# Optimization experiments

Measured on AMD Instinct MI355X. Metric: run time of the kernel, lower is better.

The kernel has to match this reference:

```python
import jax, jax.numpy as jnp
import numpy as np

H = 256   # hidden_dim
K = 4     # number of z_layer Linears
T = 8192  # number of permutation trees (Z-nodes) in the batch
C = 16    # children (leaf indices) per tree
N = 200000  # rows in batch.x node-feature table


def setup_inputs() -> dict:
    key = jax.random.key(0)
    ks = jax.random.split(key, 6)
    x = jax.random.normal(ks[0], (N, H), dtype=jnp.float32)
    leaf_idx = jax.random.randint(ks[1], (T, C), 0, N)
    # z_layer: k Linears (y = x @ W + b), z_final_layer: one Linear
    scale = 1.0 / np.sqrt(H)
    Wz = jax.random.uniform(ks[2], (K, H, H), dtype=jnp.float32, minval=-scale, maxval=scale)
    bz = jax.random.uniform(ks[3], (K, H), dtype=jnp.float32, minval=-scale, maxval=scale)
    Wzf = jax.random.uniform(ks[4], (H, H), dtype=jnp.float32, minval=-scale, maxval=scale)
    bzf = jax.random.uniform(ks[5], (H,), dtype=jnp.float32, minval=-scale, maxval=scale)
    return {"x": x, "Wz": Wz, "bz": bz, "Wzf": Wzf, "bzf": bzf, "leaf_idx": leaf_idx}


def reference(x, Wz, bz, Wzf, bzf, leaf_idx):
    # Batched z_layer_fn over T trees, each a Z-node over C leaf children.
    data = x[leaf_idx]                                   # [T, C, H] gather (fetch_or_produce)
    # k parallel Linears: [K, T, C, H]
    after = jnp.einsum('tch,khd->ktcd', data, Wz) + bz[:, None, None, :]
    # embedding_k[torch.roll(arange(C), shifts=k)] == roll(embedding_k, k, axis=children)
    k = after.shape[0]
    rolled_sum = after[0]
    for i in range(1, k):  # tiny fixed loop over k layers
        rolled_sum = rolled_sum + jnp.roll(after[i], i, axis=1)
    h = jax.nn.elu(rolled_sum)                           # [T, C, H]
    h = jnp.einsum('tch,hd->tcd', h, Wzf) + bzf          # z_final_layer
    out = jax.nn.elu(jnp.sum(h, axis=1))                 # sum over children, ELU -> [T, H]
    return out
```

## Files before the change

kernel.cpp:

```cpp
#include <hip/hip_runtime.h>
#include <hip/hip_bf16.h>
#include <stdint.h>

#define TREES 8192
#define HID   256
#define CH    16
#define KL    4
#define G     8
#define LDSS  264

typedef short bf16x8 __attribute__((ext_vector_type(8)));
typedef float f32x4  __attribute__((ext_vector_type(4)));

__device__ __forceinline__ unsigned short f2bf(float f) {
    unsigned u = __builtin_bit_cast(unsigned, f);
    u += 0x7FFFu + ((u >> 16) & 1u);
    return (unsigned short)(u >> 16);
}
__device__ __forceinline__ float elu1(float x) {
    return x > 0.f ? x : (__expf(x) - 1.f);
}

__global__ void prep_transpose(const float* __restrict__ Wz,
                               const float* __restrict__ Wzf,
                               unsigned short* __restrict__ WzT,
                               unsigned short* __restrict__ WzfT) {
    __shared__ unsigned short ts[64][65];
    const int k  = blockIdx.z;
    const int h0 = blockIdx.x * 64;
    const int d0 = blockIdx.y * 64;
    const float* src = (k < KL) ? (Wz + (k << 16)) : Wzf;
    unsigned short* dst = (k < KL) ? (WzT + (k << 16)) : WzfT;
    const int tid = threadIdx.x;
    const int jc  = tid & 63;
    #pragma unroll
    for (int r = 0; r < 16; ++r) {
        int i = r * 4 + (tid >> 6);
        ts[jc][i] = f2bf(src[(h0 + i) * HID + d0 + jc]);
    }
    __syncthreads();
    #pragma unroll
    for (int r = 0; r < 16; ++r) {
        int jl = r * 4 + (tid >> 6);
        dst[(d0 + jl) * HID + h0 + jc] = ts[jl][jc];
    }
}

__global__ void prep_bzsum(const float* __restrict__ bz, float* __restrict__ bzsum) {
    int d = threadIdx.x;
    float s = 0.f;
    #pragma unroll
    for (int k = 0; k < KL; ++k) s += bz[k * HID + d];
    bzsum[d] = s;
}

__global__ __launch_bounds__(256, 2) void ptree_kernel(
    const float* __restrict__ x,
    const int* __restrict__ leaf,
    const float* __restrict__ bzf,
    const unsigned short* __restrict__ WzT,
    const unsigned short* __restrict__ WzfT,
    const float* __restrict__ bzsum,
    float* __restrict__ out,
    int nrows)
{
    __shared__ __align__(16) unsigned short sh[G][CH][LDSS];
    __shared__ __align__(16) unsigned short hs[CH][LDSS];
    const int tid  = threadIdx.x;
    const int lane = tid & 63;
    const int wave = tid >> 6;
    const int t0   = blockIdx.x * G;
    const int ncol = lane & 15;
    const int quad = lane >> 4;

    #pragma unroll
    for (int i = 0; i < (G * CH * 32) / 256; ++i) {
        int cid = i * 256 + tid;
        int g   = cid >> 9;
        int row = (cid >> 5) & 15;
        int ch  = cid & 31;
        int idx = leaf[(t0 + g) * CH + row];
        idx = (idx >= 0 && idx < nrows) ? idx : 0;
        const float* src = x + (size_t)idx * HID + ch * 8;
        float4 v0 = *(const float4*)src;
        float4 v1 = *(const float4*)(src + 4);
        union { uint4 u4; unsigned short s[8]; } U;
        U.s[0] = f2bf(v0.x); U.s[1] = f2bf(v0.y);
        U.s[2] = f2bf(v0.z); U.s[3] = f2bf(v0.w);
        U.s[4] = f2bf(v1.x); U.s[5] = f2bf(v1.y);
        U.s[6] = f2bf(v1.z); U.s[7] = f2bf(v1.w);
        *(uint4*)&sh[g][row][ch * 8] = U.u4;
    }

    float bzs[4], bzfv[4];
    #pragma unroll
    for (int nt = 0; nt < 4; ++nt) {
        bzs[nt]  = bzsum[wave * 64 + nt * 16 + ncol];
        bzfv[nt] = bzf[wave * 64 + nt * 16 + ncol];
    }

    __syncthreads();

    f32x4 acc1[G][4];
    #pragma unroll
    for (int g = 0; g < G; ++g)
        #pragma unroll
        for (int nt = 0; nt < 4; ++nt) acc1[g][nt] = f32x4{0.f, 0.f, 0.f, 0.f};

    const unsigned short* wz_base = WzT + (wave * 64 + ncol) * HID + quad * 8;
    bf16x8 bc[4], bn[4];
    #pragma unroll
    for (int nt = 0; nt < 4; ++nt)
        bc[nt] = *(const bf16x8*)(wz_base + nt * 16 * HID);

    #pragma unroll 2
    for (int s = 0; s < KL * 8; ++s) {
        const int sn = (s < KL * 8 - 1) ? s + 1 : s;
        const unsigned short* pn = wz_base + (sn >> 3) * 65536 + (sn & 7) * 32;
        #pragma unroll
        for (int nt = 0; nt < 4; ++nt)
            bn[nt] = *(const bf16x8*)(pn + nt * 16 * HID);
        const int k    = s >> 3;
        const int kt   = s & 7;
        const int arow = (ncol - k) & 15;
        #pragma unroll
        for (int g = 0; g < G; ++g) {
            bf16x8 a = *(const bf16x8*)&sh[g][arow][kt * 32 + quad * 8];
            #pragma unroll
            for (int nt = 0; nt < 4; ++nt)
                acc1[g][nt] = __builtin_amdgcn_mfma_f32_16x16x32_bf16(a, bc[nt], acc1[g][nt], 0, 0, 0);
        }
        #pragma unroll
        for (int nt = 0; nt < 4; ++nt) bc[nt] = bn[nt];
    }

    #pragma unroll
    for (int g = 0; g < G; ++g)
        #pragma unroll
        for (int nt = 0; nt < 4; ++nt) {
            float s = 0.f;
            #pragma unroll
            for (int r = 0; r < 4; ++r) s += elu1(acc1[g][nt][r] + bzs[nt]);
            s += __shfl_xor(s, 16);
            s += __shfl_xor(s, 32);
            if (quad == 0) hs[g][wave * 64 + nt * 16 + ncol] = f2bf(s);
        }

    __syncthreads();

    f32x4 acc2[4];
    #pragma unroll
    for (int nt = 0; nt < 4; ++nt) acc2[nt] = f32x4{0.f, 0.f, 0.f, 0.f};

    const unsigned short* wzf_base = WzfT + (wave * 64 + ncol) * HID + quad * 8;
    #pragma unroll 2
    for (int kt = 0; kt < 8; ++kt) {
        bf16x8 a = *(const bf16x8*)&hs[ncol & 7][kt * 32 + quad * 8];
        if (ncol >= 8) a = bf16x8{0, 0, 0, 0, 0, 0, 0, 0};
        #pragma unroll
        for (int nt = 0; nt < 4; ++nt) {
            bf16x8 b = *(const bf16x8*)(wzf_base + nt * 16 * HID + kt * 32);
            acc2[nt] = __builtin_amdgcn_mfma_f32_16x16x32_bf16(a, b, acc2[nt], 0, 0, 0);
        }
    }

    #pragma unroll
    for (int nt = 0; nt < 4; ++nt)
        #pragma unroll
        for (int r = 0; r < 4; ++r) {
            int tree = quad * 4 + r;
            if (tree < G) {
                float v = elu1(acc2[nt][r] + 16.f * bzfv[nt]);
                out[(size_t)(t0 + tree) * HID + wave * 64 + nt * 16 + ncol] = v;
            }
        }
}

extern "C" void kernel_launch(void* const* d_in, const int* in_sizes, int n_in,
                              void* d_out, int out_size, void* d_ws, size_t ws_size,
                              hipStream_t stream) {
    (void)out_size; (void)ws_size;
    const void* p_x = nullptr; const void* p_Wz = nullptr; const void* p_bz = nullptr;
    const void* p_Wzf = nullptr; const void* p_bzf = nullptr; const void* p_leaf = nullptr;
    for (int i = 0; i < n_in; ++i) {
        switch (in_sizes[i]) {
            case 200000 * 256:   p_x    = d_in[i]; break;
            case KL * 256 * 256: p_Wz   = d_in[i]; break;
            case KL * 256:       p_bz   = d_in[i]; break;
            case 256 * 256:      p_Wzf  = d_in[i]; break;
            case 256:            p_bzf  = d_in[i]; break;
            case TREES * CH:     p_leaf = d_in[i]; break;
        }
    }
    const float* x    = (const float*)p_x;
    const float* Wz   = (const float*)p_Wz;
    const float* bz   = (const float*)p_bz;
    const float* Wzf  = (const float*)p_Wzf;
    const float* bzf  = (const float*)p_bzf;
    const int*   leaf = (const int*)p_leaf;

    unsigned short* WzT  = (unsigned short*)d_ws;
    unsigned short* WzfT = WzT + KL * HID * HID;
    float*          bzsum = (float*)(WzfT + HID * HID);

    dim3 tg(4, 4, KL + 1);
    prep_transpose<<<tg, 256, 0, stream>>>(Wz, Wzf, WzT, WzfT);
    prep_bzsum<<<1, HID, 0, stream>>>(bz, bzsum);
    ptree_kernel<<<TREES / G, 256, 0, stream>>>(x, leaf, bzf, WzT, WzfT, bzsum,
                                                (float*)d_out, 200000);
}
```

Before: 349.5 us.

## Halve trees per block, alias hidden buffer into gather LDS, batch gather loads

Cuts trees per block from 8 to 4 and raises the launch-bounds occupancy hint to 4 blocks per CU. The stage-two hidden buffer now reuses the gather LDS region, which needs an extra barrier after the first MFMA loop. The gather first loads all leaf indices, then issues global loads in batches of four before converting them to bf16, giving more memory-level parallelism. In exchange, each block now reads the weights for only half as many trees, doubling total weight traffic from L2, and the second GEMM uses only 4 of its 16 MFMA rows.

```diff
diff --git a/kernel.cpp b/kernel.cpp
--- a/kernel.cpp
+++ b/kernel.cpp
@@ -6,7 +6,7 @@
 #define HID   256
 #define CH    16
 #define KL    4
-#define G     8
+#define G     4
 #define LDSS  264
 
 typedef short bf16x8 __attribute__((ext_vector_type(8)));
@@ -54,7 +54,7 @@
     bzsum[d] = s;
 }
 
-__global__ __launch_bounds__(256, 2) void ptree_kernel(
+__global__ __launch_bounds__(256, 4) void ptree_kernel(
     const float* __restrict__ x,
     const int* __restrict__ leaf,
     const float* __restrict__ bzf,
@@ -65,7 +65,8 @@
     int nrows)
 {
     __shared__ __align__(16) unsigned short sh[G][CH][LDSS];
-    __shared__ __align__(16) unsigned short hs[CH][LDSS];
+    unsigned short (*hs)[LDSS] = (unsigned short (*)[LDSS])&sh[0][0][0];
+
     const int tid  = threadIdx.x;
     const int lane = tid & 63;
     const int wave = tid >> 6;
@@ -73,23 +74,38 @@
     const int ncol = lane & 15;
     const int quad = lane >> 4;
 
-    #pragma unroll
-    for (int i = 0; i < (G * CH * 32) / 256; ++i) {
+    int idxs[8];
+    #pragma unroll
+    for (int i = 0; i < 8; ++i) {
         int cid = i * 256 + tid;
-        int g   = cid >> 9;
-        int row = (cid >> 5) & 15;
-        int ch  = cid & 31;
-        int idx = leaf[(t0 + g) * CH + row];
-        idx = (idx >= 0 && idx < nrows) ? idx : 0;
-        const float* src = x + (size_t)idx * HID + ch * 8;
-        float4 v0 = *(const float4*)src;
-        float4 v1 = *(const float4*)(src + 4);
-        union { uint4 u4; unsigned short s[8]; } U;
-        U.s[0] = f2bf(v0.x); U.s[1] = f2bf(v0.y);
-        U.s[2] = f2bf(v0.z); U.s[3] = f2bf(v0.w);
-        U.s[4] = f2bf(v1.x); U.s[5] = f2bf(v1.y);
-        U.s[6] = f2bf(v1.z); U.s[7] = f2bf(v1.w);
-        *(uint4*)&sh[g][row][ch * 8] = U.u4;
+        int idx = leaf[(t0 + (cid >> 9)) * CH + ((cid >> 5) & 15)];
+        idxs[i] = (idx >= 0 && idx < nrows) ? idx : 0;
+    }
+    #pragma unroll
+    for (int b = 0; b < 2; ++b) {
+        float4 v0[4], v1[4];
+        #pragma unroll
+        for (int j = 0; j < 4; ++j) {
+            int i = b * 4 + j;
+            int ch = (i * 256 + tid) & 31;
+            const float* src = x + (size_t)idxs[i] * HID + ch * 8;
+            v0[j] = *(const float4*)src;
+            v1[j] = *(const float4*)(src + 4);
+        }
+        #pragma unroll
+        for (int j = 0; j < 4; ++j) {
+            int i = b * 4 + j;
+            int cid = i * 256 + tid;
+            int g   = cid >> 9;
+            int row = (cid >> 5) & 15;
+            int ch  = cid & 31;
+            union { uint4 u4; unsigned short s[8]; } U;
+            U.s[0] = f2bf(v0[j].x); U.s[1] = f2bf(v0[j].y);
+            U.s[2] = f2bf(v0[j].z); U.s[3] = f2bf(v0[j].w);
+            U.s[4] = f2bf(v1[j].x); U.s[5] = f2bf(v1[j].y);
+            U.s[6] = f2bf(v1[j].z); U.s[7] = f2bf(v1[j].w);
+            *(uint4*)&sh[g][row][ch * 8] = U.u4;
+        }
     }
 
     float bzs[4], bzfv[4];
@@ -133,6 +149,8 @@
         #pragma unroll
         for (int nt = 0; nt < 4; ++nt) bc[nt] = bn[nt];
     }
+
+    __syncthreads();
 
     #pragma unroll
     for (int g = 0; g < G; ++g)
@@ -155,8 +173,8 @@
     const unsigned short* wzf_base = WzfT + (wave * 64 + ncol) * HID + quad * 8;
     #pragma unroll 2
     for (int kt = 0; kt < 8; ++kt) {
-        bf16x8 a = *(const bf16x8*)&hs[ncol & 7][kt * 32 + quad * 8];
-        if (ncol >= 8) a = bf16x8{0, 0, 0, 0, 0, 0, 0, 0};
+        bf16x8 a = *(const bf16x8*)&hs[ncol & 3][kt * 32 + quad * 8];
+        if (ncol >= G) a = bf16x8{0, 0, 0, 0, 0, 0, 0, 0};
         #pragma unroll
         for (int nt = 0; nt < 4; ++nt) {
             bf16x8 b = *(const bf16x8*)(wzf_base + nt * 16 * HID + kt * 32);
@@ -164,16 +182,15 @@
         }
     }
 
-    #pragma unroll
-    for (int nt = 0; nt < 4; ++nt)
-        #pragma unroll
-        for (int r = 0; r < 4; ++r) {
-            int tree = quad * 4 + r;
-            if (tree < G) {
+    if (quad == 0) {
+        #pragma unroll
+        for (int nt = 0; nt < 4; ++nt)
+            #pragma unroll
+            for (int r = 0; r < 4; ++r) {
                 float v = elu1(acc2[nt][r] + 16.f * bzfv[nt]);
-                out[(size_t)(t0 + tree) * HID + wave * 64 + nt * 16 + ncol] = v;
+                out[(size_t)(t0 + r) * HID + wave * 64 + nt * 16 + ncol] = v;
             }
-        }
+    }
 }
 
 extern "C" void kernel_launch(void* const* d_in, const int* in_sizes, int n_in,
```

Measured after the change: 407.1 us. 1.16x slower.
